# Kernel tuning notes

Hardware: AMD Instinct MI355X
Metric: run time of the kernel (lower is better)

## Reference

```python
import jax, jax.numpy as jnp
import numpy as np

SEQ_LEN = 4096
D_MODEL = 1024
OUT_DIM = 1024
KERNEL = 256
STRIDE = 16
NUM_HEADS = 16


def _p(key, *shape):
    return jax.random.normal(key, shape, dtype=jnp.float32) * 0.02


def setup_inputs() -> dict:
    key = jax.random.key(0)
    ks = jax.random.split(key, 12)
    return {
        "path": jax.random.normal(ks[0], (SEQ_LEN, D_MODEL), dtype=jnp.float32),
        # sliding_module (nn.MultiheadAttention, embed_dim=D_MODEL)
        "w_in1": _p(ks[1], 3 * D_MODEL, D_MODEL),
        "b_in1": jnp.zeros((3 * D_MODEL,), jnp.float32),
        "w_out1": _p(ks[2], D_MODEL, D_MODEL),
        "b_out1": jnp.zeros((D_MODEL,), jnp.float32),
        # linear_module
        "w_lin": _p(ks[3], OUT_DIM, D_MODEL),
        "b_lin": jnp.zeros((OUT_DIM,), jnp.float32),
        # accum_module (embed_dim=OUT_DIM)
        "w_in2": _p(ks[4], 3 * OUT_DIM, OUT_DIM),
        "b_in2": jnp.zeros((3 * OUT_DIM,), jnp.float32),
        "w_out2": _p(ks[5], OUT_DIM, OUT_DIM),
        "b_out2": jnp.zeros((OUT_DIM,), jnp.float32),
    }


def _mha(q, k, v, w_in, b_in, w_out, b_out, num_heads):
    """torch nn.MultiheadAttention math (dropout=0). q,k,v: [..., L, E]."""
    E = q.shape[-1]
    Dh = E // num_heads
    wq, wk, wv = jnp.split(w_in, 3, axis=0)
    bq, bk, bv = jnp.split(b_in, 3)
    def heads(t):
        return t.reshape(t.shape[:-1] + (num_heads, Dh))
    qh = heads(q @ wq.T + bq)
    kh = heads(k @ wk.T + bk)
    vh = heads(v @ wv.T + bv)
    scale = 1.0 / np.sqrt(Dh).astype(np.float32)
    att = jax.nn.softmax(jnp.einsum("...qhd,...khd->...hqk", qh, kh) * scale, axis=-1)
    out = jnp.einsum("...hqk,...khd->...qhd", att, vh)
    out = out.reshape(out.shape[:-2] + (E,))
    return out @ w_out.T + b_out


def reference(path, w_in1, b_in1, w_out1, b_out1, w_lin, b_lin,
              w_in2, b_in2, w_out2, b_out2):
    seq_len = path.shape[-2]
    slices_num = (seq_len - KERNEL) // STRIDE
    # overlapping windows: [slices_num, KERNEL, D_MODEL]
    idx = jnp.arange(slices_num)[:, None] * STRIDE + jnp.arange(KERNEL)[None, :]
    x = path[idx]
    # batched self-attention over windows
    x = _mha(x, x, x, w_in1, b_in1, w_out1, b_out1, NUM_HEADS)
    x = jax.nn.relu(x @ w_lin.T + b_lin)  # [slices_num, KERNEL, OUT_DIM]
    # sequential recurrent attention accumulation
    def step(cum_att, xi):
        new = _mha(xi, cum_att, cum_att, w_in2, b_in2, w_out2, b_out2, NUM_HEADS)
        return new, None
    cum_att, _ = jax.lax.scan(step, x[0], x[1:])
    return cum_att  # [KERNEL, OUT_DIM]
```

## Files before the change

kernel.cpp:

```cpp
#include <hip/hip_runtime.h>
#include <math.h>

#define D_MODEL 1024
#define N_WIN   240
#define TOK     256
#define NH      16
#define DH      64
#define CHUNK   8
#define NCHUNK  30
#define WIN     ((size_t)TOK * D_MODEL)

typedef unsigned short ushort_t;
typedef unsigned long long ull_t;
typedef __attribute__((ext_vector_type(8))) short short8;
typedef __attribute__((ext_vector_type(4))) float floatx4;

__device__ __forceinline__ ushort_t f2bf(float f) {
    unsigned u = __float_as_uint(f);
    unsigned lsb = (u >> 16) & 1u;
    u += 0x7fffu + lsb;
    return (ushort_t)(u >> 16);
}

__device__ __forceinline__ void st2_wt(ushort_t* p, ushort_t v) {
    unsigned vv = v;
    asm volatile("global_store_short %0, %1, off sc1"
                 :: "v"(p), "v"(vv) : "memory");
}
__device__ __forceinline__ void st8_wt(ushort_t* p, ushort4 v) {
    ull_t dv = (ull_t)((unsigned)v.x | ((unsigned)v.y << 16))
             | ((ull_t)((unsigned)v.z | ((unsigned)v.w << 16)) << 32);
    asm volatile("global_store_dwordx2 %0, %1, off sc1"
                 :: "v"(p), "v"(dv) : "memory");
}
__device__ __forceinline__ void rel_drain() {
    asm volatile("s_waitcnt vmcnt(0)" ::: "memory");
}

#define GLDS(g, l) __builtin_amdgcn_global_load_lds( \
    (const __attribute__((address_space(1))) unsigned int*)(g), \
    (__attribute__((address_space(3))) unsigned int*)(l), 16, 0, 0)

__device__ __forceinline__ void help_bar(unsigned* base, int g, unsigned s)
{
    rel_drain();
    __syncthreads();
    if (threadIdx.x == 0) {
        unsigned old = __hip_atomic_fetch_add(base + 1024 + g * 32, 1u,
                __ATOMIC_RELAXED, __HIP_MEMORY_SCOPE_AGENT);
        if (old == 8u * s - 1u) {
            unsigned r = __hip_atomic_fetch_add(base + 1800, 1u,
                    __ATOMIC_RELAXED, __HIP_MEMORY_SCOPE_AGENT);
            if (r == 24u * s - 1u)
                __hip_atomic_store(base + 1832, s, __ATOMIC_RELAXED,
                                   __HIP_MEMORY_SCOPE_AGENT);
        }
        while (__hip_atomic_load(base + 1832, __ATOMIC_RELAXED,
                                 __HIP_MEMORY_SCOPE_AGENT) < s)
            __builtin_amdgcn_s_sleep(1);
    }
    __syncthreads();
}

__global__ __launch_bounds__(256) void cast_bf_k(
    const float* __restrict__ s, ushort_t* __restrict__ d, int n)
{
    int i = (blockIdx.x * 256 + threadIdx.x) * 4;
    if (i >= n) return;
    float4 v = *(const float4*)(s + i);
    ushort4 o;
    o.x = f2bf(v.x); o.y = f2bf(v.y); o.z = f2bf(v.z); o.w = f2bf(v.w);
    *(ushort4*)(d + i) = o;
}

__global__ __launch_bounds__(256) void transpose_k(
    const ushort_t* __restrict__ src, ushort_t* __restrict__ dst)
{
    __shared__ ushort_t t[64][65];
    const int bx = blockIdx.x * 64, by = blockIdx.y * 64;
    const int c = threadIdx.x & 63, r0 = threadIdx.x >> 6;
#pragma unroll
    for (int k = 0; k < 16; ++k) {
        int r = r0 + k * 4;
        t[r][c] = src[(size_t)(by + r) * 1024 + bx + c];
    }
    __syncthreads();
#pragma unroll
    for (int k = 0; k < 16; ++k) {
        int r = r0 + k * 4;
        dst[(size_t)(bx + r) * 1024 + by + c] = t[c][r];
    }
}

__global__ __launch_bounds__(256) void bc_k(
    const float* __restrict__ w_in2, const float* __restrict__ b_in2,
    const float* __restrict__ b_out2, float* __restrict__ bc)
{
    int n = blockIdx.x * 256 + threadIdx.x;
    const float* row = w_in2 + (size_t)(1024 + n) * 1024;
    float s = b_in2[1024 + n];
    for (int j = 0; j < 1024; j += 4) {
        float4 w = *(const float4*)(row + j);
        float4 b = *(const float4*)(b_out2 + j);
        s += w.x * b.x + w.y * b.y + w.z * b.z + w.w * b.w;
    }
    bc[n] = s;
}

template<bool GATHER, bool WT>
__device__ __forceinline__ void gemm_core(
    ushort_t* As, ushort_t* Bs,
    const ushort_t* __restrict__ A, int lda, int w0,
    const ushort_t* __restrict__ W, const float* __restrict__ bias,
    ushort_t* __restrict__ Cb, float* __restrict__ Cf, int ldc,
    int K, int m0, int n0, int co, int relu)
{
    const int tid = threadIdx.x;
    const int wave = tid >> 6, lane = tid & 63;
    const int wm = wave & 1, wn = wave >> 1;

    int r0 = m0 + (tid >> 2), r1 = r0 + 64;
    if (GATHER) {
        r0 = (w0 + (r0 >> 8)) * 16 + (r0 & 255);
        r1 = (w0 + (r1 >> 8)) * 16 + (r1 & 255);
    }
    const int kcol = (tid & 3) * 8;
    const ushort_t* gA0 = A + (size_t)r0 * lda + kcol;
    const ushort_t* gA1 = A + (size_t)r1 * lda + kcol;
    const ushort_t* pW  = W + (size_t)n0 * K;
    const ushort_t* gB0 = pW + (size_t)(tid >> 2) * K + kcol;
    const ushort_t* gB1 = gB0 + (size_t)64 * K;
    ushort_t* lA = As + wave * 512;
    ushort_t* lB = Bs + wave * 512;

    floatx4 acc[4][4];
#pragma unroll
    for (int i = 0; i < 4; ++i)
#pragma unroll
        for (int j = 0; j < 4; ++j) acc[i][j] = (floatx4){0.f, 0.f, 0.f, 0.f};

    const int fr = lane & 15, fk = (lane >> 4) * 8;
    const int arow = (wm * 64 + fr) * 32 + fk;
    const int brow = (wn * 64 + fr) * 32 + fk;

    for (int k0 = 0; k0 < K; k0 += 32) {
        GLDS(gA0 + k0, lA);
        GLDS(gA1 + k0, lA + 2048);
        GLDS(gB0 + k0, lB);
        GLDS(gB1 + k0, lB + 2048);
        __syncthreads();
        short8 a[4], b[4];
#pragma unroll
        for (int mi = 0; mi < 4; ++mi) a[mi] = *(const short8*)&As[arow + mi * 512];
#pragma unroll
        for (int ni = 0; ni < 4; ++ni) b[ni] = *(const short8*)&Bs[brow + ni * 512];
#pragma unroll
        for (int mi = 0; mi < 4; ++mi)
#pragma unroll
            for (int ni = 0; ni < 4; ++ni)
                acc[mi][ni] = __builtin_amdgcn_mfma_f32_16x16x32_bf16(
                    a[mi], b[ni], acc[mi][ni], 0, 0, 0);
        __syncthreads();
    }

    const int crq = (lane >> 4) * 4;
    const int ccol = lane & 15;
#pragma unroll
    for (int mi = 0; mi < 4; ++mi) {
#pragma unroll
        for (int ni = 0; ni < 4; ++ni) {
            int lc = wn * 64 + ni * 16 + ccol;
            float bz = bias[n0 + lc];
#pragma unroll
            for (int rg = 0; rg < 4; ++rg) {
                int row = m0 + wm * 64 + mi * 16 + crq + rg;
                float v = acc[mi][ni][rg] + bz;
                if (relu) v = fmaxf(v, 0.f);
                size_t off = (size_t)row * ldc + co + lc;
                if (Cb) {
                    if (WT) st2_wt(Cb + off, f2bf(v));
                    else    Cb[off] = f2bf(v);
                }
                if (Cf) Cf[off] = v;
            }
        }
    }
}

__global__ __launch_bounds__(256) void gemm_bf_k(
    const ushort_t* __restrict__ A, int lda,
    const ushort_t* __restrict__ W, const float* __restrict__ bias,
    ushort_t* __restrict__ Cb, float* __restrict__ Cf, int ldc,
    int K, int relu)
{
    __shared__ ushort_t As[128 * 32];
    __shared__ ushort_t Bs[128 * 32];
    gemm_core<false, false>(As, Bs, A, lda, 0, W, bias, Cb, Cf, ldc, K,
                            blockIdx.y * 128, blockIdx.x * 128, blockIdx.x * 128, relu);
}

__global__ __launch_bounds__(256) void gemm_qkv_k(
    const ushort_t* __restrict__ path_bf, const ushort_t* __restrict__ W,
    const float* __restrict__ bias, ushort_t* __restrict__ Cb, int w0)
{
    __shared__ ushort_t As[128 * 32];
    __shared__ ushort_t Bs[128 * 32];
    gemm_core<true, false>(As, Bs, path_bf, 1024, w0, W, bias, Cb, nullptr, 3072, 1024,
                           blockIdx.y * 128, blockIdx.x * 128, blockIdx.x * 128, 0);
}

#define PLD 260
#define VLD 132

struct AttnShared {
    ushort_t P[64 * PLD];
    ushort_t VT[64 * VLD];
    float    l[64];
};

__device__ void attn_body(AttnShared& sh,
    const ushort_t* __restrict__ qkv, ushort_t* __restrict__ ao,
    int rs, int h, int b)
{
    const ushort_t* base = qkv + (size_t)b * TOK * 3072;
    const ushort_t* Q = base;
    const ushort_t* K = base + 1024;
    const ushort_t* V = base + 2048;
    ushort_t* O = ao + (size_t)b * TOK * 1024;
    const int ldq = 3072, ldkv = 3072, ldo = 1024;
    const int tid = threadIdx.x;
    const int wave = tid >> 6, lane = tid & 63;
    const int fr = lane & 15, q = lane >> 4, fk = q * 8;
    const ushort_t* Qh = Q + (size_t)(rs * 64) * ldq + h * 64;
    const ushort_t* Kh = K + h * 64;
    const ushort_t* Vh = V + h * 64;
    const int m0 = wave * 16;

    floatx4 s[16];
#pragma unroll
    for (int nt = 0; nt < 16; ++nt) s[nt] = (floatx4){0.f, 0.f, 0.f, 0.f};
#pragma unroll
    for (int kc = 0; kc < 64; kc += 32) {
        short8 a = *(const short8*)(Qh + (size_t)(m0 + fr) * ldq + kc + fk);
#pragma unroll
        for (int nt = 0; nt < 16; ++nt) {
            short8 b2 = *(const short8*)(Kh + (size_t)(nt * 16 + fr) * ldkv + kc + fk);
            s[nt] = __builtin_amdgcn_mfma_f32_16x16x32_bf16(a, b2, s[nt], 0, 0, 0);
        }
    }

    float rmax[4] = {-INFINITY, -INFINITY, -INFINITY, -INFINITY};
#pragma unroll
    for (int nt = 0; nt < 16; ++nt)
#pragma unroll
        for (int rg = 0; rg < 4; ++rg) rmax[rg] = fmaxf(rmax[rg], s[nt][rg]);
#pragma unroll
    for (int d = 1; d < 16; d <<= 1)
#pragma unroll
        for (int rg = 0; rg < 4; ++rg)
            rmax[rg] = fmaxf(rmax[rg], __shfl_xor(rmax[rg], d));

    float rsum[4] = {0.f, 0.f, 0.f, 0.f};
#pragma unroll
    for (int nt = 0; nt < 16; ++nt) {
#pragma unroll
        for (int rg = 0; rg < 4; ++rg) {
            float p = __expf((s[nt][rg] - rmax[rg]) * 0.125f);
            rsum[rg] += p;
            sh.P[(m0 + q * 4 + rg) * PLD + nt * 16 + fr] = f2bf(p);
        }
    }
#pragma unroll
    for (int d = 1; d < 16; d <<= 1)
#pragma unroll
        for (int rg = 0; rg < 4; ++rg) rsum[rg] += __shfl_xor(rsum[rg], d);
    if (fr == 0) {
#pragma unroll
        for (int rg = 0; rg < 4; ++rg) sh.l[m0 + q * 4 + rg] = rsum[rg];
    }
    __syncthreads();

    floatx4 o[4];
#pragma unroll
    for (int i = 0; i < 4; ++i) o[i] = (floatx4){0.f, 0.f, 0.f, 0.f};

#pragma unroll
    for (int half = 0; half < 2; ++half) {
        {
            int r = tid & 127, cp = tid >> 7;
            const ushort_t* vrow = Vh + (size_t)(half * 128 + r) * ldkv + cp * 32;
#pragma unroll
            for (int c = 0; c < 4; ++c) {
                uint4 pk = *(const uint4*)(vrow + c * 8);
                int d0 = cp * 32 + c * 8;
                sh.VT[(d0 + 0) * VLD + r] = (ushort_t)(pk.x & 0xffff);
                sh.VT[(d0 + 1) * VLD + r] = (ushort_t)(pk.x >> 16);
                sh.VT[(d0 + 2) * VLD + r] = (ushort_t)(pk.y & 0xffff);
                sh.VT[(d0 + 3) * VLD + r] = (ushort_t)(pk.y >> 16);
                sh.VT[(d0 + 4) * VLD + r] = (ushort_t)(pk.z & 0xffff);
                sh.VT[(d0 + 5) * VLD + r] = (ushort_t)(pk.z >> 16);
                sh.VT[(d0 + 6) * VLD + r] = (ushort_t)(pk.w & 0xffff);
                sh.VT[(d0 + 7) * VLD + r] = (ushort_t)(pk.w >> 16);
            }
        }
        __syncthreads();
#pragma unroll
        for (int ks = 0; ks < 4; ++ks) {
            short8 a = *(const short8*)&sh.P[(m0 + fr) * PLD + half * 128 + ks * 32 + fk];
#pragma unroll
            for (int nt2 = 0; nt2 < 4; ++nt2) {
                short8 b2 = *(const short8*)&sh.VT[(nt2 * 16 + fr) * VLD + ks * 32 + fk];
                o[nt2] = __builtin_amdgcn_mfma_f32_16x16x32_bf16(a, b2, o[nt2], 0, 0, 0);
            }
        }
        __syncthreads();
    }

    float linv[4];
#pragma unroll
    for (int rg = 0; rg < 4; ++rg) linv[rg] = 1.f / sh.l[m0 + q * 4 + rg];
#pragma unroll
    for (int nt2 = 0; nt2 < 4; ++nt2)
#pragma unroll
        for (int rg = 0; rg < 4; ++rg) {
            int row = rs * 64 + m0 + q * 4 + rg;
            st2_wt(O + (size_t)row * ldo + h * 64 + nt2 * 16 + fr,
                   f2bf(o[nt2][rg] * linv[rg]));
        }
    __syncthreads();
}

__global__ __launch_bounds__(256) void attn_mfma_k(
    const ushort_t* __restrict__ qkv, ushort_t* __restrict__ ao)
{
    __shared__ AttnShared sh;
    attn_body(sh, qkv, ao, blockIdx.x, blockIdx.y, blockIdx.z);
}

#define KLD 76
#define TLD 264

struct ScanSmem {
    union {
        struct { ushort_t Ab[3][4096]; ushort_t Wb[4][8192]; } st;
        struct { ushort_t Kl[256 * KLD]; ushort_t Vt[64 * TLD];
                 ushort_t P[64 * TLD]; } at;
    };
};

__device__ __forceinline__ void stage_A(
    const ushort_t* __restrict__ A64, int k0, ushort_t* __restrict__ Ad,
    int wave, int lane)
{
#pragma unroll
    for (int t = 0; t < 2; ++t) {
        int j = wave * 128 + t * 64 + lane;
        int row = j >> 3;
        int blk = (j & 7) ^ (row & 7);
        GLDS(A64 + (size_t)row * 1024 + k0 + blk * 8,
             Ad + wave * 1024 + t * 512);
    }
}

__device__ __forceinline__ void stage_W(
    const ushort_t* __restrict__ Wsel, int h, int k0,
    ushort_t* __restrict__ Wd, int wave, int lane)
{
#pragma unroll
    for (int t = 0; t < 4; ++t) {
        int j = wave * 256 + t * 64 + lane;
        int r = j >> 3;
        int blk = (j & 7) ^ (r & 7);
        int n = ((r >> 6) << 10) + h * 64 + (r & 63);
        GLDS(Wsel + (size_t)n * 1024 + k0 + blk * 8,
             Wd + wave * 2048 + t * 512);
    }
}

__device__ void scan_body(
    ScanSmem& sm, int h, int rs, int g,
    const ushort_t* __restrict__ Qchunk, int i0, int w0, int nsteps,
    const ushort_t* __restrict__ x0, ushort_t* __restrict__ AOb,
    ushort_t* __restrict__ KVx,
    const ushort_t* __restrict__ Wkv, const float* __restrict__ bkv,
    const ushort_t* __restrict__ Wc, const float* __restrict__ bc,
    unsigned* __restrict__ bar, unsigned s0)
{
    const int tid = threadIdx.x;
    const int wave = tid >> 6, lane = tid & 63;
    const int fr = lane & 15, q = lane >> 4, fk = q * 8;
    const int m0g = rs * 64 + wave * 16;

    const int dbofs = (wave < 2 ? 0 : 1024) + h * 64 + (wave & 1) * 32;
    float bK1[2], bC1[2];
#pragma unroll
    for (int nt = 0; nt < 2; ++nt) {
        bK1[nt] = bkv[dbofs + nt * 16 + fr];
        bC1[nt] = bc[dbofs + nt * 16 + fr];
    }

    ushort_t* Kl = sm.at.Kl;
    ushort_t* Vt = sm.at.Vt;
    ushort_t* P  = sm.at.P;

    short8 qf0, qf1;
    {
        const int i = i0;
        const ushort_t* Wsel0 = (i == 1) ? Wkv : Wc;
        stage_W(Wsel0, h, 0,  sm.st.Wb[0], wave, lane);
        stage_W(Wsel0, h, 64, sm.st.Wb[1], wave, lane);
        const ushort_t* Qrow = Qchunk + (size_t)(i - w0) * WIN
            + (size_t)(m0g + fr) * 1024 + h * 64;
        qf0 = *(const short8*)(Qrow);
        qf1 = *(const short8*)(Qrow + 32);
        const ushort_t* Asrc0 = (i == 1) ? x0
            : AOb + (size_t)((i - 1) & 7) * WIN;
        stage_A(Asrc0 + (size_t)rs * 64 * 1024, 0, sm.st.Ab[0], wave, lane);
    }

    unsigned s = s0;
    for (int t0 = 0; t0 < nsteps; ++t0, ++s) {
        const int i = i0 + t0;
        const ushort_t* Asrc = (i == 1) ? x0
            : AOb + (size_t)((i - 1) & 7) * WIN;
        const ushort_t* Wsel = (i == 1) ? Wkv : Wc;
        const ushort_t* A64 = Asrc + (size_t)rs * 64 * 1024;
        ushort_t* KVs = KVx + (size_t)(i & 7) * (NH * 32768) + h * 32768;

        floatx4 acc[4][2];
#pragma unroll
        for (int mt = 0; mt < 4; ++mt)
#pragma unroll
            for (int nt = 0; nt < 2; ++nt)
                acc[mt][nt] = (floatx4){0.f, 0.f, 0.f, 0.f};

#pragma unroll 1
        for (int t = 0; t < 16; ++t) {
            if (t < 15)
                stage_A(A64, (t + 1) * 64, sm.st.Ab[(t + 1) % 3], wave, lane);
            if (t < 14)
                stage_W(Wsel, h, (t + 2) * 64, sm.st.Wb[(t + 2) & 3], wave, lane);
            if (t == 15)
                asm volatile("s_waitcnt vmcnt(0)" ::: "memory");
            else
                asm volatile("s_waitcnt vmcnt(6)" ::: "memory");
            __builtin_amdgcn_s_barrier();
            const ushort_t* Ac  = sm.st.Ab[t % 3];
            const ushort_t* Wc_ = sm.st.Wb[t & 3];
#pragma unroll
            for (int kh = 0; kh < 2; ++kh) {
                const int pb = (((kh << 2) + q) ^ (fr & 7)) * 8;
                short8 a[4];
#pragma unroll
                for (int mt = 0; mt < 4; ++mt)
                    a[mt] = *(const short8*)&Ac[(mt * 16 + fr) * 64 + pb];
#pragma unroll
                for (int nt = 0; nt < 2; ++nt) {
                    short8 b = *(const short8*)
                        &Wc_[(wave * 32 + nt * 16 + fr) * 64 + pb];
#pragma unroll
                    for (int mt = 0; mt < 4; ++mt)
                        acc[mt][nt] = __builtin_amdgcn_mfma_f32_16x16x32_bf16(
                            a[mt], b, acc[mt][nt], 0, 0, 0);
                }
            }
        }
        __builtin_amdgcn_s_barrier();
        ushort_t* Kx = KVs;
        ushort_t* Vx = KVs + 16384;
#pragma unroll
        for (int mt = 0; mt < 4; ++mt) {
#pragma unroll
            for (int nt = 0; nt < 2; ++nt) {
                const float bz = (i == 1) ? bK1[nt] : bC1[nt];
                const int d = (wave & 1) * 32 + nt * 16 + fr;
                if (wave < 2) {
#pragma unroll
                    for (int rg = 0; rg < 4; ++rg) {
                        const int key = rs * 64 + mt * 16 + q * 4 + rg;
                        st2_wt(Kx + key * 64 + d, f2bf(acc[mt][nt][rg] + bz));
                    }
                } else {
                    ushort4 pv;
                    pv.x = f2bf(acc[mt][nt][0] + bz);
                    pv.y = f2bf(acc[mt][nt][1] + bz);
                    pv.z = f2bf(acc[mt][nt][2] + bz);
                    pv.w = f2bf(acc[mt][nt][3] + bz);
                    st8_wt(Vx + d * 256 + rs * 64 + mt * 16 + q * 4, pv);
                }
            }
        }
        rel_drain();
        __syncthreads();
        if (tid == 0)
            __hip_atomic_fetch_add(bar + 384 + h * 32, 1u,
                    __ATOMIC_RELAXED, __HIP_MEMORY_SCOPE_AGENT);

#pragma unroll
        for (int mt = 0; mt < 4; ++mt) {
#pragma unroll
            for (int nt = 0; nt < 2; ++nt) {
                const float bz = (i == 1) ? bK1[nt] : bC1[nt];
                const int d = (wave & 1) * 32 + nt * 16 + fr;
                if (wave < 2) {
#pragma unroll
                    for (int rg = 0; rg < 4; ++rg) {
                        const int key = rs * 64 + mt * 16 + q * 4 + rg;
                        Kl[key * KLD + d] = f2bf(acc[mt][nt][rg] + bz);
                    }
                } else {
                    ushort4 pv;
                    pv.x = f2bf(acc[mt][nt][0] + bz);
                    pv.y = f2bf(acc[mt][nt][1] + bz);
                    pv.z = f2bf(acc[mt][nt][2] + bz);
                    pv.w = f2bf(acc[mt][nt][3] + bz);
                    *(ushort4*)&Vt[d * TLD + rs * 64 + mt * 16 + q * 4] = pv;
                }
            }
        }
        if (tid == 0) {
            while (__hip_atomic_load(bar + 384 + h * 32, __ATOMIC_RELAXED,
                                     __HIP_MEMORY_SCOPE_AGENT) < 4u * s)
                __builtin_amdgcn_s_sleep(1);
        }
        __syncthreads();

        {
            if (wave != rs) {
                const ushort_t* kr = Kx + tid * 64;
                uint4 kb4[8];
#pragma unroll
                for (int s8 = 0; s8 < 8; ++s8)
                    kb4[s8] = *(const uint4*)(kr + s8 * 8);
                const int kp = (tid >> 4) & 3;
#pragma unroll
                for (int s8 = 0; s8 < 8; ++s8) {
                    int ks = (s8 + kp) & 7;
                    *(uint4*)&Kl[tid * KLD + ks * 8] = kb4[ks];
                }
            }
            const int vd = tid >> 2, vq = tid & 3;
            if (vq != rs) {
                const ushort_t* vr = Vx + vd * 256 + vq * 64;
                uint4 vb4[8];
#pragma unroll
                for (int s8 = 0; s8 < 8; ++s8)
                    vb4[s8] = *(const uint4*)(vr + s8 * 8);
                const int vp = vq << 1;
#pragma unroll
                for (int s8 = 0; s8 < 8; ++s8) {
                    int vs = (s8 + vp) & 7;
                    *(uint4*)&Vt[vd * TLD + vq * 64 + vs * 8] = vb4[vs];
                }
            }
        }
        __syncthreads();

        ushort_t* AOcur = AOb + (size_t)(i & 7) * WIN;
        {
            const int pl0 = wave * 16;
            floatx4 sc[16];
#pragma unroll
            for (int nt = 0; nt < 16; ++nt) sc[nt] = (floatx4){0.f, 0.f, 0.f, 0.f};
#pragma unroll
            for (int kc = 0; kc < 64; kc += 32) {
                short8 a = (kc == 0) ? qf0 : qf1;
#pragma unroll
                for (int nt = 0; nt < 16; ++nt) {
                    short8 b = *(const short8*)&Kl[(nt * 16 + fr) * KLD + kc + fk];
                    sc[nt] = __builtin_amdgcn_mfma_f32_16x16x32_bf16(
                        a, b, sc[nt], 0, 0, 0);
                }
            }
            float rmax[4] = {-INFINITY, -INFINITY, -INFINITY, -INFINITY};
#pragma unroll
            for (int nt = 0; nt < 16; ++nt)
#pragma unroll
                for (int rg = 0; rg < 4; ++rg) rmax[rg] = fmaxf(rmax[rg], sc[nt][rg]);
#pragma unroll
            for (int d = 1; d < 16; d <<= 1)
#pragma unroll
                for (int rg = 0; rg < 4; ++rg)
                    rmax[rg] = fmaxf(rmax[rg], __shfl_xor(rmax[rg], d));
            float rsum[4] = {0.f, 0.f, 0.f, 0.f};
#pragma unroll
            for (int nt = 0; nt < 16; ++nt) {
#pragma unroll
                for (int rg = 0; rg < 4; ++rg) {
                    float p = __expf((sc[nt][rg] - rmax[rg]) * 0.125f);
                    rsum[rg] += p;
                    P[(pl0 + q * 4 + rg) * TLD + nt * 16 + fr] = f2bf(p);
                }
            }
#pragma unroll
            for (int d = 1; d < 16; d <<= 1)
#pragma unroll
                for (int rg = 0; rg < 4; ++rg) rsum[rg] += __shfl_xor(rsum[rg], d);

            floatx4 o[4];
#pragma unroll
            for (int nt = 0; nt < 4; ++nt) o[nt] = (floatx4){0.f, 0.f, 0.f, 0.f};
#pragma unroll
            for (int kt = 0; kt < 8; ++kt) {
                short8 a = *(const short8*)&P[(pl0 + fr) * TLD + kt * 32 + fk];
#pragma unroll
                for (int nt = 0; nt < 4; ++nt) {
                    short8 b = *(const short8*)&Vt[(nt * 16 + fr) * TLD + kt * 32 + fk];
                    o[nt] = __builtin_amdgcn_mfma_f32_16x16x32_bf16(
                        a, b, o[nt], 0, 0, 0);
                }
            }
            float linv[4];
#pragma unroll
            for (int rg = 0; rg < 4; ++rg) linv[rg] = 1.f / rsum[rg];
#pragma unroll
            for (int nt = 0; nt < 4; ++nt)
#pragma unroll
                for (int rg = 0; rg < 4; ++rg) {
                    int row = m0g + q * 4 + rg;
                    st2_wt(AOcur + (size_t)row * 1024 + h * 64 + nt * 16 + fr,
                           f2bf(o[nt][rg] * linv[rg]));
                }
        }

        rel_drain();
        __syncthreads();
        if (tid == 0) {
            unsigned old = __hip_atomic_fetch_add(bar + g * 32, 1u,
                    __ATOMIC_RELAXED, __HIP_MEMORY_SCOPE_AGENT);
            if (old == 8u * s - 1u) {
                unsigned r = __hip_atomic_fetch_add(bar + 256, 1u,
                        __ATOMIC_RELAXED, __HIP_MEMORY_SCOPE_AGENT);
                if (r == 8u * s - 1u)
                    __hip_atomic_store(bar + 288, s, __ATOMIC_RELAXED,
                                       __HIP_MEMORY_SCOPE_AGENT);
            }
        }
        const bool more = (t0 + 1 < nsteps);
        if (more) {
            stage_W(Wc, h, 0,  sm.st.Wb[0], wave, lane);
            stage_W(Wc, h, 64, sm.st.Wb[1], wave, lane);
            const ushort_t* Qrow = Qchunk + (size_t)(i + 1 - w0) * WIN
                + (size_t)(m0g + fr) * 1024 + h * 64;
            qf0 = *(const short8*)(Qrow);
            qf1 = *(const short8*)(Qrow + 32);
        }
        if (tid == 0 && more) {
            while (__hip_atomic_load(bar + 288, __ATOMIC_RELAXED,
                                     __HIP_MEMORY_SCOPE_AGENT) < s)
                __builtin_amdgcn_s_sleep(1);
        }
        __syncthreads();
        if (more)
            stage_A(AOb + (size_t)(i & 7) * WIN + (size_t)rs * 64 * 1024, 0,
                    sm.st.Ab[0], wave, lane);
    }
}

struct GemmSmem { ushort_t As[128 * 32]; ushort_t Bs[128 * 32]; };
union FusedSmem { ScanSmem scan; GemmSmem gem; AttnShared att; };

__global__ __launch_bounds__(256, 1) void fused_k(
    const ushort_t* __restrict__ Qchunk, int i0, int w0, int nsteps,
    const ushort_t* __restrict__ x0, ushort_t* __restrict__ AOb,
    ushort_t* __restrict__ KVx,
    const ushort_t* __restrict__ Wkv, const float* __restrict__ bkv,
    const ushort_t* __restrict__ Wc, const float* __restrict__ bc,
    unsigned* __restrict__ bar, unsigned s0,
    int do_help, int w0n,
    const ushort_t* __restrict__ path_bf,
    const ushort_t* __restrict__ w_in1, const float* __restrict__ b_in1,
    ushort_t* __restrict__ qkv, ushort_t* __restrict__ ao,
    ushort_t* __restrict__ ybuf,
    const ushort_t* __restrict__ w_out1, const float* __restrict__ b_out1,
    const ushort_t* __restrict__ w_lin, const float* __restrict__ b_lin,
    ushort_t* __restrict__ Xc,
    const ushort_t* __restrict__ w_in2, const float* __restrict__ b_in2,
    ushort_t* __restrict__ Qnext, unsigned hs0)
{
    __shared__ FusedSmem sm;
    const int wg = blockIdx.x;
    const int x = wg & 7, y = wg >> 3;

    if (x < 2) {
        const int scanIdx = x * 32 + y;
        const int h  = (x << 3) | (y >> 2);
        const int rs = y & 3;
        const int g  = scanIdx & 7;
        scan_body(sm.scan, h, rs, g,
                  Qchunk, i0, w0, nsteps, x0, AOb, KVx,
                  Wkv, bkv, Wc, bc, bar, s0);
        return;
    }
    if (!do_help) return;

    const int hw = (x - 2) * 32 + y;
    const int hg = hw >> 3;

    for (int t = hw; t < 384; t += 192) {
        int bx = t % 24, by = t / 24;
        gemm_core<true, true>(sm.gem.As, sm.gem.Bs, path_bf, 1024, w0n,
                              w_in1, b_in1, qkv, nullptr, 3072, 1024,
                              by * 128, bx * 128, bx * 128, 0);
    }
    help_bar(bar, hg, hs0);

    for (int t = hw; t < 512; t += 192) {
        int rs = t & 3, h = (t >> 2) & 15, b = t >> 6;
        attn_body(sm.att, qkv, ao, rs, h, b);
    }
    help_bar(bar, hg, hs0 + 1);

    for (int t = hw; t < 128; t += 192) {
        int bx = t & 7, by = t >> 3;
        gemm_core<false, true>(sm.gem.As, sm.gem.Bs, ao, 1024, 0,
                               w_out1, b_out1, ybuf, nullptr, 1024, 1024,
                               by * 128, bx * 128, bx * 128, 0);
    }
    help_bar(bar, hg, hs0 + 2);

    for (int t = hw; t < 128; t += 192) {
        int bx = t & 7, by = t >> 3;
        gemm_core<false, true>(sm.gem.As, sm.gem.Bs, ybuf, 1024, 0,
                               w_lin, b_lin, Xc, nullptr, 1024, 1024,
                               by * 128, bx * 128, bx * 128, 1);
    }
    help_bar(bar, hg, hs0 + 3);

    for (int t = hw; t < 128; t += 192) {
        int bx = t & 7, by = t >> 3;
        gemm_core<false, true>(sm.gem.As, sm.gem.Bs, Xc, 1024, 0,
                               w_in2, b_in2, Qnext, nullptr, 1024, 1024,
                               by * 128, bx * 128, bx * 128, 0);
    }
}

extern "C" void kernel_launch(void* const* d_in, const int* in_sizes, int n_in,
                              void* d_out, int out_size, void* d_ws, size_t ws_size,
                              hipStream_t stream)
{
    const float* path   = (const float*)d_in[0];
    const float* w_in1  = (const float*)d_in[1];
    const float* b_in1  = (const float*)d_in[2];
    const float* w_out1 = (const float*)d_in[3];
    const float* b_out1 = (const float*)d_in[4];
    const float* w_lin  = (const float*)d_in[5];
    const float* b_lin  = (const float*)d_in[6];
    const float* w_in2  = (const float*)d_in[7];
    const float* b_in2  = (const float*)d_in[8];
    const float* w_out2 = (const float*)d_in[9];
    const float* b_out2 = (const float*)d_in[10];
    float* out = (float*)d_out;

    unsigned* bar = (unsigned*)d_ws;
    float* bc      = (float*)d_ws + 2048;
    float* zerosf  = bc + 2048;
    ushort_t* ws = (ushort_t*)d_ws + 16384;
    ushort_t* path_bf  = ws;
    ushort_t* w_in1_bf = path_bf  + (size_t)4096 * 1024;
    ushort_t* w_out1_bf= w_in1_bf + (size_t)3072 * 1024;
    ushort_t* w_lin_bf = w_out1_bf+ (size_t)1024 * 1024;
    ushort_t* w_in2_bf = w_lin_bf + (size_t)1024 * 1024;
    ushort_t* w_out2_bf= w_in2_bf + (size_t)3072 * 1024;
    ushort_t* WoT_bf   = w_out2_bf+ (size_t)1024 * 1024;
    ushort_t* Wc_bf    = WoT_bf   + (size_t)1024 * 1024;
    ushort_t* qkv_bf   = Wc_bf    + (size_t)2048 * 1024;
    ushort_t* ao_bf    = qkv_bf   + (size_t)2048 * 3072;
    ushort_t* ybuf_bf  = ao_bf    + (size_t)2048 * 1024;
    ushort_t* Xbuf     = ybuf_bf  + (size_t)2048 * 1024;
    ushort_t* Qb0      = Xbuf     + (size_t)2048 * 1024;
    ushort_t* Qb1      = Qb0      + (size_t)2048 * 1024;
    ushort_t* AOb      = Qb1      + (size_t)2048 * 1024;
    ushort_t* x0buf    = AOb + 8 * WIN;
    ushort_t* dummy    = x0buf + WIN;
    ushort_t* KVx      = dummy + WIN;
    ushort_t* Qb[2] = {Qb0, Qb1};

    hipMemsetAsync(bar, 0, 8192, stream);
    hipMemsetAsync(zerosf, 0, 1024 * sizeof(float), stream);

    cast_bf_k<<<4096, 256, 0, stream>>>(path,  path_bf,  4096 * 1024);
    cast_bf_k<<<3072, 256, 0, stream>>>(w_in1, w_in1_bf, 3072 * 1024);
    cast_bf_k<<<1024, 256, 0, stream>>>(w_out1, w_out1_bf, 1024 * 1024);
    cast_bf_k<<<1024, 256, 0, stream>>>(w_lin, w_lin_bf, 1024 * 1024);
    cast_bf_k<<<3072, 256, 0, stream>>>(w_in2, w_in2_bf, 3072 * 1024);
    cast_bf_k<<<1024, 256, 0, stream>>>(w_out2, w_out2_bf, 1024 * 1024);

    transpose_k<<<dim3(16, 16), 256, 0, stream>>>(w_out2_bf, WoT_bf);
    bc_k<<<8, 256, 0, stream>>>(w_in2, b_in2, b_out2, bc);
    gemm_bf_k<<<dim3(8, 16), 256, 0, stream>>>(
        w_in2_bf + (size_t)1024 * 1024, 1024, WoT_bf, zerosf,
        Wc_bf, nullptr, 1024, 1024, 0);

    gemm_qkv_k<<<dim3(24, 16), 256, 0, stream>>>(
        path_bf, w_in1_bf, b_in1, qkv_bf, 0);
    attn_mfma_k<<<dim3(4, NH, CHUNK), 256, 0, stream>>>(qkv_bf, ao_bf);
    gemm_bf_k<<<dim3(8, 16), 256, 0, stream>>>(
        ao_bf, 1024, w_out1_bf, b_out1, ybuf_bf, nullptr, 1024, 1024, 0);
    gemm_bf_k<<<dim3(8, 16), 256, 0, stream>>>(
        ybuf_bf, 1024, w_lin_bf, b_lin, Xbuf, nullptr, 1024, 1024, 1);
    gemm_bf_k<<<dim3(8, 16), 256, 0, stream>>>(
        Xbuf, 1024, w_in2_bf, b_in2, Qb[0], nullptr, 1024, 1024, 0);
    (void)hipMemcpyAsync(x0buf, Xbuf, WIN * sizeof(ushort_t),
                         hipMemcpyDeviceToDevice, stream);

    unsigned sbase = 1;
    for (int c = 0; c < NCHUNK; ++c) {
        int w0 = c * CHUNK;
        int i0 = (c == 0) ? 1 : w0;
        int nsteps = (c == 0) ? CHUNK - 1 : CHUNK;
        int do_help = (c + 1 < NCHUNK) ? 1 : 0;
        int w0n = (c + 1) * CHUNK;
        unsigned hs0 = (unsigned)(c * 4 + 1);
        const ushort_t* Qcur = Qb[c & 1];
        ushort_t* Qnext = Qb[(c + 1) & 1];
        const ushort_t* x0P = x0buf;
        ushort_t* AObP = AOb;
        ushort_t* KVxP = KVx;
        const ushort_t* WkvP = w_in2_bf + (size_t)1024 * 1024;
        const float* bkvP = b_in2 + 1024;
        const ushort_t* WcP = Wc_bf;
        const float* bcP = bc;
        unsigned* barP = bar;
        unsigned sb = sbase;
        const ushort_t* pathP = path_bf;
        const ushort_t* win1P = w_in1_bf;
        const float* bin1P = b_in1;
        ushort_t* qkvP = qkv_bf;
        ushort_t* aoP = ao_bf;
        ushort_t* ybufP = ybuf_bf;
        const ushort_t* wout1P = w_out1_bf;
        const float* bout1P = b_out1;
        const ushort_t* wlinP = w_lin_bf;
        const float* blinP = b_lin;
        ushort_t* XP = Xbuf;
        const ushort_t* win2P = w_in2_bf;
        const float* bin2P = b_in2;
        void* args[] = {&Qcur, &i0, &w0, &nsteps, &x0P, &AObP, &KVxP,
                        &WkvP, &bkvP, &WcP, &bcP, &barP, &sb,
                        &do_help, &w0n, &pathP, &win1P, &bin1P,
                        &qkvP, &aoP, &ybufP, &wout1P, &bout1P,
                        &wlinP, &blinP, &XP, &win2P, &bin2P, &Qnext, &hs0};
        hipLaunchCooperativeKernel((void*)fused_k, dim3(256), dim3(256),
                                   args, 0, stream);
        sbase += (unsigned)nsteps;
    }

    gemm_bf_k<<<dim3(8, 2), 256, 0, stream>>>(
        AOb + (size_t)((N_WIN - 1) & 7) * WIN, 1024, w_out2_bf, b_out2,
        dummy, out, 1024, 1024, 0);
}
```

Before: 6.207 ms.

## Double K-step in scan GEMM and replace global barrier with per-row-slice counters

The scan projection GEMM now stages 128-wide K slices (two 64-wide halves) per iteration with 3-stage buffers for A and W, halving the number of workgroup barriers per step. The two-level global barrier across all 64 scan workgroups is replaced by a per-row-slice counter that waits only for the 16 head workgroups sharing the same rs. This cuts synchronisation latency on the sequential scan critical path, at the cost of more LDS use and a dependency assumption that the next step reads only its own row slice of the previous output. That assumption may not hold, because keys and values span all rows.

```diff
diff --git a/kernel.cpp b/kernel.cpp
--- a/kernel.cpp
+++ b/kernel.cpp
@@ -342,7 +342,7 @@
 
 struct ScanSmem {
     union {
-        struct { ushort_t Ab[3][4096]; ushort_t Wb[4][8192]; } st;
+        struct { ushort_t Ab[3][8192]; ushort_t Wb[3][16384]; } st;
         struct { ushort_t Kl[256 * KLD]; ushort_t Vt[64 * TLD];
                  ushort_t P[64 * TLD]; } at;
     };
@@ -378,7 +378,7 @@
 }
 
 __device__ void scan_body(
-    ScanSmem& sm, int h, int rs, int g,
+    ScanSmem& sm, int h, int rs,
     const ushort_t* __restrict__ Qchunk, int i0, int w0, int nsteps,
     const ushort_t* __restrict__ x0, ushort_t* __restrict__ AOb,
     ushort_t* __restrict__ KVx,
@@ -408,14 +408,15 @@
         const int i = i0;
         const ushort_t* Wsel0 = (i == 1) ? Wkv : Wc;
         stage_W(Wsel0, h, 0,  sm.st.Wb[0], wave, lane);
-        stage_W(Wsel0, h, 64, sm.st.Wb[1], wave, lane);
+        stage_W(Wsel0, h, 64, sm.st.Wb[0] + 8192, wave, lane);
         const ushort_t* Qrow = Qchunk + (size_t)(i - w0) * WIN
             + (size_t)(m0g + fr) * 1024 + h * 64;
         qf0 = *(const short8*)(Qrow);
         qf1 = *(const short8*)(Qrow + 32);
         const ushort_t* Asrc0 = (i == 1) ? x0
             : AOb + (size_t)((i - 1) & 7) * WIN;
-        stage_A(Asrc0 + (size_t)rs * 64 * 1024, 0, sm.st.Ab[0], wave, lane);
+        stage_A(Asrc0 + (size_t)rs * 64 * 1024, 0,  sm.st.Ab[0], wave, lane);
+        stage_A(Asrc0 + (size_t)rs * 64 * 1024, 64, sm.st.Ab[0] + 4096, wave, lane);
     }
 
     unsigned s = s0;
@@ -435,33 +436,39 @@
                 acc[mt][nt] = (floatx4){0.f, 0.f, 0.f, 0.f};
 
 #pragma unroll 1
-        for (int t = 0; t < 16; ++t) {
-            if (t < 15)
-                stage_A(A64, (t + 1) * 64, sm.st.Ab[(t + 1) % 3], wave, lane);
-            if (t < 14)
-                stage_W(Wsel, h, (t + 2) * 64, sm.st.Wb[(t + 2) & 3], wave, lane);
-            if (t == 15)
+        for (int t = 0; t < 8; ++t) {
+            if (t < 7) {
+                stage_A(A64, (t + 1) * 128,      sm.st.Ab[(t + 1) % 3], wave, lane);
+                stage_A(A64, (t + 1) * 128 + 64, sm.st.Ab[(t + 1) % 3] + 4096, wave, lane);
+                stage_W(Wsel, h, (t + 1) * 128,      sm.st.Wb[(t + 1) % 3], wave, lane);
+                stage_W(Wsel, h, (t + 1) * 128 + 64, sm.st.Wb[(t + 1) % 3] + 8192, wave, lane);
+                asm volatile("s_waitcnt vmcnt(12)" ::: "memory");
+            } else {
                 asm volatile("s_waitcnt vmcnt(0)" ::: "memory");
-            else
-                asm volatile("s_waitcnt vmcnt(6)" ::: "memory");
+            }
             __builtin_amdgcn_s_barrier();
             const ushort_t* Ac  = sm.st.Ab[t % 3];
-            const ushort_t* Wc_ = sm.st.Wb[t & 3];
-#pragma unroll
-            for (int kh = 0; kh < 2; ++kh) {
-                const int pb = (((kh << 2) + q) ^ (fr & 7)) * 8;
-                short8 a[4];
-#pragma unroll
-                for (int mt = 0; mt < 4; ++mt)
-                    a[mt] = *(const short8*)&Ac[(mt * 16 + fr) * 64 + pb];
-#pragma unroll
-                for (int nt = 0; nt < 2; ++nt) {
-                    short8 b = *(const short8*)
-                        &Wc_[(wave * 32 + nt * 16 + fr) * 64 + pb];
+            const ushort_t* Wc_ = sm.st.Wb[t % 3];
+#pragma unroll
+            for (int sub = 0; sub < 2; ++sub) {
+                const ushort_t* Acs = Ac  + sub * 4096;
+                const ushort_t* Wcs = Wc_ + sub * 8192;
+#pragma unroll
+                for (int kh = 0; kh < 2; ++kh) {
+                    const int pb = (((kh << 2) + q) ^ (fr & 7)) * 8;
+                    short8 a[4];
 #pragma unroll
                     for (int mt = 0; mt < 4; ++mt)
-                        acc[mt][nt] = __builtin_amdgcn_mfma_f32_16x16x32_bf16(
-                            a[mt], b, acc[mt][nt], 0, 0, 0);
+                        a[mt] = *(const short8*)&Acs[(mt * 16 + fr) * 64 + pb];
+#pragma unroll
+                    for (int nt = 0; nt < 2; ++nt) {
+                        short8 b = *(const short8*)
+                            &Wcs[(wave * 32 + nt * 16 + fr) * 64 + pb];
+#pragma unroll
+                        for (int mt = 0; mt < 4; ++mt)
+                            acc[mt][nt] = __builtin_amdgcn_mfma_f32_16x16x32_bf16(
+                                a[mt], b, acc[mt][nt], 0, 0, 0);
+                    }
                 }
             }
         }
@@ -625,35 +632,30 @@
 
         rel_drain();
         __syncthreads();
-        if (tid == 0) {
-            unsigned old = __hip_atomic_fetch_add(bar + g * 32, 1u,
+        if (tid == 0)
+            __hip_atomic_fetch_add(bar + 960 + rs * 16, 1u,
                     __ATOMIC_RELAXED, __HIP_MEMORY_SCOPE_AGENT);
-            if (old == 8u * s - 1u) {
-                unsigned r = __hip_atomic_fetch_add(bar + 256, 1u,
-                        __ATOMIC_RELAXED, __HIP_MEMORY_SCOPE_AGENT);
-                if (r == 8u * s - 1u)
-                    __hip_atomic_store(bar + 288, s, __ATOMIC_RELAXED,
-                                       __HIP_MEMORY_SCOPE_AGENT);
-            }
-        }
         const bool more = (t0 + 1 < nsteps);
         if (more) {
             stage_W(Wc, h, 0,  sm.st.Wb[0], wave, lane);
-            stage_W(Wc, h, 64, sm.st.Wb[1], wave, lane);
+            stage_W(Wc, h, 64, sm.st.Wb[0] + 8192, wave, lane);
             const ushort_t* Qrow = Qchunk + (size_t)(i + 1 - w0) * WIN
                 + (size_t)(m0g + fr) * 1024 + h * 64;
             qf0 = *(const short8*)(Qrow);
             qf1 = *(const short8*)(Qrow + 32);
         }
         if (tid == 0 && more) {
-            while (__hip_atomic_load(bar + 288, __ATOMIC_RELAXED,
-                                     __HIP_MEMORY_SCOPE_AGENT) < s)
+            while (__hip_atomic_load(bar + 960 + rs * 16, __ATOMIC_RELAXED,
+                                     __HIP_MEMORY_SCOPE_AGENT) < 16u * s)
                 __builtin_amdgcn_s_sleep(1);
         }
         __syncthreads();
-        if (more)
-            stage_A(AOb + (size_t)(i & 7) * WIN + (size_t)rs * 64 * 1024, 0,
-                    sm.st.Ab[0], wave, lane);
+        if (more) {
+            const ushort_t* An = AOb + (size_t)(i & 7) * WIN
+                + (size_t)rs * 64 * 1024;
+            stage_A(An, 0,  sm.st.Ab[0], wave, lane);
+            stage_A(An, 64, sm.st.Ab[0] + 4096, wave, lane);
+        }
     }
 }
 
@@ -683,11 +685,9 @@
     const int x = wg & 7, y = wg >> 3;
 
     if (x < 2) {
-        const int scanIdx = x * 32 + y;
         const int h  = (x << 3) | (y >> 2);
         const int rs = y & 3;
-        const int g  = scanIdx & 7;
-        scan_body(sm.scan, h, rs, g,
+        scan_body(sm.scan, h, rs,
                   Qchunk, i0, w0, nsteps, x0, AOb, KVx,
                   Wkv, bkv, Wc, bc, bar, s0);
         return;
```

New measurement: 6.010 ms, median of 2. 3.2% less time.
